# Performance work log

Measured on AMD Instinct MI355X. Metric: run time of the kernel, lower is better.

Reference implementation:

```python
import jax, jax.numpy as jnp
import numpy as np
from jax import lax

# --- fixed architecture (from init_kwargs) ---
S = 2048          # seq_len
HID = 2048        # hidden size
NH = 16           # num value heads == num key heads (v_per_k = 1)
DK = 128          # key head dim
DV = 128          # value head dim
K = 4             # depthwise conv kernel size
CS = 64           # chunk size
NC = S // CS      # number of chunks
KEY_DIM = NH * DK
VAL_DIM = NH * DV
CONV_DIM = 2 * KEY_DIM + VAL_DIM
EPS = 1e-6        # rms_norm_eps


def setup_inputs() -> dict:
    key = jax.random.key(0)
    ks = jax.random.split(key, 10)
    def n(k, shape, s=1.0):
        return s * jax.random.normal(k, shape, dtype=jnp.float32)
    return {
        'hidden_in':     n(ks[0], (1, S, HID)),
        'in_proj_qkv_w': n(ks[1], (CONV_DIM, HID), 0.02),
        'in_proj_z_w':   n(ks[2], (VAL_DIM, HID), 0.02),
        'in_proj_b_w':   n(ks[3], (NH, HID), 0.02),
        'in_proj_a_w':   n(ks[4], (NH, HID), 0.02),
        'out_proj_w':    n(ks[5], (HID, VAL_DIM), 0.02),
        'conv_w':        n(ks[6], (CONV_DIM, 1, K), 0.2),
        'dt_bias':       n(ks[7], (NH,), 0.1),
        'A_log':         n(ks[8], (NH,), 0.1),
        'norm_w':        1.0 + n(ks[9], (DV,), 0.02),
    }


def _l2norm(x):
    return x * lax.rsqrt(jnp.sum(x * x, axis=-1, keepdims=True) + 1e-6)


def _chunk_gated_delta_rule(q, k, v, g, beta):
    # q,k: (1,NH,S,DK)  v: (1,NH,S,DV)  g,beta: (1,NH,S)
    scale = 1.0 / np.sqrt(DK).astype(np.float32)
    q = q * scale
    kb = k * beta[..., None]
    vb = v * beta[..., None]
    q = q.reshape(1, NH, NC, CS, DK)
    k = k.reshape(1, NH, NC, CS, DK)
    v = v.reshape(1, NH, NC, CS, DV)
    kb = kb.reshape(1, NH, NC, CS, DK)
    vb = vb.reshape(1, NH, NC, CS, DV)
    g = jnp.cumsum(g.reshape(1, NH, NC, CS), axis=-1)

    gd = jnp.minimum(g[..., :, None] - g[..., None, :], 10.0)       # (1,NH,NC,CS,CS)
    tril = jnp.tril(jnp.ones((CS, CS), bool))                        # incl diag
    strict_low = jnp.tril(jnp.ones((CS, CS), bool), -1)
    dm = jnp.where(tril, jnp.exp(gd), 0.0)                           # decay mask

    # L = strictly-lower part of -(k_beta k^T) * decay_mask
    L = jnp.where(strict_low, -jnp.einsum('bhcid,bhcjd->bhcij', kb, k) * dm, 0.0)
    eye = jnp.eye(CS, dtype=q.dtype)

    # 64-step Neumann series inverting (I - L), with clamping as in source
    def neumann(attn, _):
        attn = eye + jnp.einsum('bhcij,bhcjk->bhcik', L, attn)
        return jnp.clip(attn, -1000.0, 1000.0), None
    attn, _ = lax.scan(neumann, jnp.broadcast_to(eye, L.shape), None, length=CS)

    value = jnp.einsum('bhcij,bhcjd->bhcid', attn, vb)
    kcd = jnp.einsum('bhcij,bhcjd->bhcid', attn, kb * jnp.exp(g)[..., None])

    xs = tuple(jnp.moveaxis(t, 2, 0) for t in (q, k, value, kcd, g, dm))

    def step(state, xs_i):  # state: (1,NH,DK,DV)
        qi, ki, vi, kcdi, gi, dmi = xs_i  # chunk tensors (1,NH,CS,...)
        ai = jnp.where(tril, jnp.einsum('bhid,bhjd->bhij', qi, ki) * dmi, 0.0)
        v_new = vi - jnp.einsum('bhid,bhdv->bhiv', kcdi, state)
        out_i = (jnp.einsum('bhid,bhdv->bhiv', qi * jnp.exp(gi)[..., None], state)
                 + jnp.einsum('bhij,bhjv->bhiv', ai, v_new))
        g_last = gi[..., -1:]                                        # (1,NH,1)
        state = (state * jnp.exp(g_last)[..., None]
                 + jnp.einsum('bhid,bhiv->bhdv', ki * jnp.exp(g_last - gi)[..., None], v_new))
        return state, out_i

    state0 = jnp.zeros((1, NH, DK, DV), q.dtype)
    last_state, outs = lax.scan(step, state0, xs)                    # outs: (NC,1,NH,CS,DV)
    core = jnp.moveaxis(outs, 0, 2).reshape(1, NH, S, DV)
    return core, last_state


def _forward(hidden_in, qkv_w, z_w, b_w, a_w, o_w, conv_w, dt_bias, A_log, norm_w):
    mixed = jnp.einsum('bsh,oh->bso', hidden_in, qkv_w)              # (1,S,CONV_DIM)
    z = jnp.einsum('bsh,oh->bso', hidden_in, z_w)                    # (1,S,VAL_DIM)
    b = jnp.einsum('bsh,oh->bso', hidden_in, b_w)                    # (1,S,NH)
    a = jnp.einsum('bsh,oh->bso', hidden_in, a_w)                    # (1,S,NH)

    # causal depthwise conv1d (padding=K-1 then truncate == left-pad K-1)
    x = jnp.pad(jnp.swapaxes(mixed, 1, 2), ((0, 0), (0, 0), (K - 1, 0)))
    conv = lax.conv_general_dilated(x, conv_w, (1,), 'VALID',
                                    dimension_numbers=('NCH', 'OIH', 'NCH'),
                                    feature_group_count=CONV_DIM)
    mixed = jax.nn.silu(jnp.swapaxes(conv, 1, 2))                    # (1,S,CONV_DIM)

    q = mixed[..., :KEY_DIM]
    k = mixed[..., KEY_DIM:2 * KEY_DIM]
    v = mixed[..., 2 * KEY_DIM:]
    q = _l2norm(jnp.swapaxes(q.reshape(1, S, NH, DK), 1, 2))         # (1,NH,S,DK)
    k = _l2norm(jnp.swapaxes(k.reshape(1, S, NH, DK), 1, 2))
    v = jnp.swapaxes(v.reshape(1, S, NH, DV), 1, 2)                  # (1,NH,S,DV)
    beta = jnp.swapaxes(jax.nn.sigmoid(b), 1, 2)                     # (1,NH,S)
    g = jnp.swapaxes(-jnp.exp(A_log) * jax.nn.softplus(a + dt_bias), 1, 2)

    core, _ = _chunk_gated_delta_rule(q, k, v, g, beta)              # (1,NH,S,DV)

    core_f = jnp.swapaxes(core, 1, 2).reshape(-1, DV)                # (S*NH, DV)
    z_f = z.reshape(-1, DV)
    # ANE rmsnorm trick == plain RMSNorm: x / sqrt(mean(x^2)+eps)
    xn = core_f * lax.rsqrt(jnp.mean(core_f * core_f, axis=-1, keepdims=True) + EPS) * norm_w
    out = (xn * jax.nn.silu(z_f)).reshape(1, S, VAL_DIM)
    return jnp.einsum('bsv,hv->bsh', out, o_w)


def reference(hidden_in, in_proj_qkv_w, in_proj_z_w, in_proj_b_w, in_proj_a_w,
              out_proj_w, conv_w, dt_bias, A_log, norm_w):
    return _forward(hidden_in, in_proj_qkv_w, in_proj_z_w, in_proj_b_w, in_proj_a_w,
                    out_proj_w, conv_w, dt_bias, A_log, norm_w)
```

## Files before the change

kernel.cpp:

```cpp
#include <hip/hip_runtime.h>
#include <math.h>

#define S_LEN 2048
#define HID 2048
#define NH 16
#define DK 128
#define DV 128
#define CS 64
#define NC 32
#define KEY_DIM 2048
#define VAL_DIM 2048
#define CONV_DIM 6144
#define QSCALE 0.08838834764831845f

typedef unsigned short u16;
typedef unsigned int u32;
typedef __bf16 bf16x8 __attribute__((ext_vector_type(8)));
typedef float f32x4 __attribute__((ext_vector_type(4)));

__device__ __forceinline__ float sigmoidf_(float x){ return 1.f/(1.f+expf(-x)); }
__device__ __forceinline__ u16 f2bf(float x){
  u32 u = __float_as_uint(x);
  return (u16)((u + 0x7fffu + ((u>>16)&1u)) >> 16);
}

constexpr size_t OFF_HIDBF  = 0;
constexpr size_t OFF_QKVWBF = 2097152;
constexpr size_t OFF_ZWBF   = 8388608;
constexpr size_t OFF_OWBF   = 10485760;
constexpr size_t OFF_GATED  = 12582912;
constexpr size_t OFF_MIXED  = 14680064;
constexpr size_t OFF_CONVO  = 27262976;
constexpr size_t OFF_Z      = 39845888;
constexpr size_t OFF_BRAW   = 44040192;
constexpr size_t OFF_ARAW   = 44072960;
constexpr size_t OFF_BETA   = 44105728;
constexpr size_t OFF_G      = 44138496;
constexpr size_t OFF_KCD    = 44171264;
constexpr size_t OFF_AI     = 48365568;
constexpr size_t OFF_SALL   = 50462720;
constexpr size_t OFF_CORE   = 58851328;
constexpr size_t OFF_AT     = OFF_MIXED;
constexpr size_t OFF_BM     = 0;
constexpr size_t OFF_BAPART = OFF_MIXED;

__global__ __launch_bounds__(256) void k_cast8(const float* __restrict__ in,
                                               u16* __restrict__ out, int n8)
{
  int i = blockIdx.x*256 + threadIdx.x;
  if (i >= n8) return;
  const float4 a = *(const float4*)(in + (size_t)i*8);
  const float4 b = *(const float4*)(in + (size_t)i*8 + 4);
  uint4 o;
  o.x = (u32)f2bf(a.x) | ((u32)f2bf(a.y)<<16);
  o.y = (u32)f2bf(a.z) | ((u32)f2bf(a.w)<<16);
  o.z = (u32)f2bf(b.x) | ((u32)f2bf(b.y)<<16);
  o.w = (u32)f2bf(b.z) | ((u32)f2bf(b.w)<<16);
  *(uint4*)(out + (size_t)i*8) = o;
}

__device__ __forceinline__ void gload16(const u16* g, u16* l){
  __builtin_amdgcn_global_load_lds(
      (__attribute__((address_space(1))) void*)(void*)g,
      (__attribute__((address_space(3))) void*)l, 16, 0, 0);
}

__global__ __launch_bounds__(256) void gemm_bf(const u16* __restrict__ A,
    const u16* __restrict__ B, float* __restrict__ C, int M, int N, int Kd)
{
  __shared__ u16 As[128*32];
  __shared__ u16 Bs[128*32];
  const int tid = threadIdx.x;
  const int w = tid>>6, lane = tid&63;
  const int wr = w>>1, wc = w&1;
  const int row0 = blockIdx.y*128, col0 = blockIdx.x*128;

  f32x4 acc[4][4] = {};

  const int sr = lane>>2;
  const int sk = (lane&3)*8;
  const u16* Ag0 = A + (size_t)(row0 + (2*w  )*16 + sr)*Kd + sk;
  const u16* Ag1 = A + (size_t)(row0 + (2*w+1)*16 + sr)*Kd + sk;
  const u16* Bg0 = B + (size_t)(col0 + (2*w  )*16 + sr)*Kd + sk;
  const u16* Bg1 = B + (size_t)(col0 + (2*w+1)*16 + sr)*Kd + sk;
  u16* Al0 = &As[(2*w  )*16*32];
  u16* Al1 = &As[(2*w+1)*16*32];
  u16* Bl0 = &Bs[(2*w  )*16*32];
  u16* Bl1 = &Bs[(2*w+1)*16*32];

  const int fr = lane&15, fc = (lane>>4)*8;
  const int arow0 = (wr*64 + fr)*32 + fc;
  const int brow0 = (wc*64 + fr)*32 + fc;

  for (int k0=0; k0<Kd; k0+=32){
    __syncthreads();
    gload16(Ag0 + k0, Al0);
    gload16(Ag1 + k0, Al1);
    gload16(Bg0 + k0, Bl0);
    gload16(Bg1 + k0, Bl1);
    __syncthreads();
    bf16x8 af[4], bfr[4];
#pragma unroll
    for (int m=0;m<4;m++) af[m]  = *(const bf16x8*)&As[arow0 + m*16*32];
#pragma unroll
    for (int n=0;n<4;n++) bfr[n] = *(const bf16x8*)&Bs[brow0 + n*16*32];
#pragma unroll
    for (int m=0;m<4;m++)
#pragma unroll
      for (int n=0;n<4;n++)
        acc[m][n] = __builtin_amdgcn_mfma_f32_16x16x32_bf16(af[m], bfr[n], acc[m][n], 0,0,0);
  }

  const int cr = (lane>>4)*4, cc = lane&15;
#pragma unroll
  for (int m=0;m<4;m++)
#pragma unroll
    for (int n=0;n<4;n++){
      float* cp = C + (size_t)(row0 + wr*64 + m*16 + cr)*N + (col0 + wc*64 + n*16 + cc);
#pragma unroll
      for (int j=0;j<4;j++) cp[(size_t)j*N] = acc[m][n][j];
    }
}

#define BA_KS 512
__global__ __launch_bounds__(256) void k_ba_part(const float* __restrict__ hid,
  const float* __restrict__ bw, const float* __restrict__ aw, float* __restrict__ part)
{
  __shared__ float Ash[32][132];
  __shared__ float Wsh[32][132];
  const int t = threadIdx.x;
  const int ty = t>>4, tx = t&15;
  const int s0 = blockIdx.x*32;
  const int k00 = blockIdx.y*BA_KS;
  float acc[2][2] = {{0.f,0.f},{0.f,0.f}};
#pragma unroll 1
  for (int kt=0; kt<BA_KS; kt+=128){
    const int k0 = k00 + kt;
    __syncthreads();
#pragma unroll
    for (int q=0;q<4;q++){
      int idx = t + q*256;
      int r = idx>>5, c4 = (idx&31)*4;
      *(float4*)&Ash[r][c4] = *(const float4*)&hid[(size_t)(s0+r)*HID + k0 + c4];
      const float* wrow = (r<16)? (bw + (size_t)r*HID) : (aw + (size_t)(r-16)*HID);
      *(float4*)&Wsh[r][c4] = *(const float4*)&wrow[k0 + c4];
    }
    __syncthreads();
#pragma unroll
    for (int kq=0;kq<32;kq++){
      float4 a0 = *(const float4*)&Ash[ty*2  ][kq*4];
      float4 a1 = *(const float4*)&Ash[ty*2+1][kq*4];
      float4 w0 = *(const float4*)&Wsh[tx*2  ][kq*4];
      float4 w1 = *(const float4*)&Wsh[tx*2+1][kq*4];
      acc[0][0] += a0.x*w0.x + a0.y*w0.y + a0.z*w0.z + a0.w*w0.w;
      acc[0][1] += a0.x*w1.x + a0.y*w1.y + a0.z*w1.z + a0.w*w1.w;
      acc[1][0] += a1.x*w0.x + a1.y*w0.y + a1.z*w0.z + a1.w*w0.w;
      acc[1][1] += a1.x*w1.x + a1.y*w1.y + a1.z*w1.z + a1.w*w1.w;
    }
  }
  float* pb = part + (size_t)blockIdx.y*S_LEN*32;
#pragma unroll
  for (int i=0;i<2;i++)
#pragma unroll
    for (int j=0;j<2;j++)
      pb[(size_t)(s0+ty*2+i)*32 + tx*2+j] = acc[i][j];
}

__global__ __launch_bounds__(256) void k_ba_red(const float* __restrict__ part,
  float* __restrict__ braw, float* __restrict__ araw)
{
  int idx = blockIdx.x*256 + threadIdx.x;
  if (idx >= S_LEN*32) return;
  float v = part[idx] + part[idx + S_LEN*32] + part[idx + 2*S_LEN*32] + part[idx + 3*S_LEN*32];
  int s = idx>>5, o = idx&31;
  if (o<16) braw[s*NH+o] = v; else araw[s*NH+(o-16)] = v;
}

__global__ __launch_bounds__(64) void k_beta_g(const float* __restrict__ braw,
  const float* __restrict__ araw, const float* __restrict__ dtb,
  const float* __restrict__ alog, float* __restrict__ beta, float* __restrict__ G)
{
  const int b = blockIdx.x;
  const int n = b & (NH-1), c = b >> 4;
  const int t = threadIdx.x;
  const int s = c*CS + t;
  float x = araw[s*NH+n] + dtb[n];
  float sp = (x > 20.f) ? x : log1pf(expf(x));
  float g = -expf(alog[n]) * sp;
#pragma unroll
  for (int off=1; off<64; off<<=1){
    float u = __shfl_up(g, off, 64);
    if (t >= off) g += u;
  }
  G[s*NH+n] = g;
  float bb = braw[s*NH+n];
  beta[s*NH+n] = 1.f/(1.f+expf(-bb));
}

__global__ __launch_bounds__(256) void k_conv(const float* __restrict__ mixed,
  const float* __restrict__ cw, float* __restrict__ convo)
{
  const int ch = blockIdx.x*256 + threadIdx.x;
  const int s0 = blockIdx.y*4;
  const float w0=cw[ch*4], w1=cw[ch*4+1], w2=cw[ch*4+2], w3=cw[ch*4+3];
  float m[7];
#pragma unroll
  for (int j=0;j<7;j++){
    int s = s0 + j - 3;
    m[j] = (s>=0) ? mixed[(size_t)s*CONV_DIM+ch] : 0.f;
  }
#pragma unroll
  for (int i=0;i<4;i++){
    float acc = m[i]*w0 + m[i+1]*w1 + m[i+2]*w2 + m[i+3]*w3;
    convo[(size_t)(s0+i)*CONV_DIM+ch] = acc*sigmoidf_(acc);
  }
}

__global__ __launch_bounds__(256) void k_l2norm(float* __restrict__ convo)
{
  const int t = threadIdx.x;
  const int lane = t & 63, w = t >> 6;
  const int s = blockIdx.x;
  const int n = blockIdx.y*4 + w;
  {
    float* q = convo + (size_t)s*CONV_DIM + n*DK;
    float q0 = q[lane], q1 = q[lane+64];
    float ss = q0*q0 + q1*q1;
#pragma unroll
    for (int m=1;m<64;m<<=1) ss += __shfl_xor(ss, m, 64);
    float r = rsqrtf(ss + 1e-6f) * QSCALE;
    q[lane] = q0*r; q[lane+64] = q1*r;
  }
  {
    float* k = convo + (size_t)s*CONV_DIM + KEY_DIM + n*DK;
    float k0 = k[lane], k1 = k[lane+64];
    float ss = k0*k0 + k1*k1;
#pragma unroll
    for (int m=1;m<64;m<<=1) ss += __shfl_xor(ss, m, 64);
    float r = rsqrtf(ss + 1e-6f);
    k[lane] = k0*r; k[lane+64] = k1*r;
  }
}

__global__ __launch_bounds__(256) void k_chunk1(float* __restrict__ convo,
  const float* __restrict__ G, const float* __restrict__ beta,
  float* __restrict__ ai_g, float* __restrict__ kcd_g)
{
  __shared__ float KT[128][76];
  __shared__ float LT[64][65];
  __shared__ float reds[4][64];
  __shared__ float Gs[64], bets[64], kes[64];
  const int c = blockIdx.x, n = blockIdx.y;
  const int t = threadIdx.x;
  const int tx = t & 15, ty = t >> 4;
  const int s0 = c*CS;
  if (t < 64){
    float gv = G[(s0+t)*NH+n], bv = beta[(s0+t)*NH+n];
    Gs[t]=gv; bets[t]=bv; kes[t]=bv*expf(gv);
  }
  __syncthreads();
  for (int idx=t; idx<CS*DK; idx+=256){
    int i = idx>>7, d = idx&127;
    KT[d][i] = convo[(size_t)(s0+i)*CONV_DIM + KEY_DIM + n*DK + d];
  }
  __syncthreads();
  {
    const int i0=ty*4, j0=tx*4;
    float l[4][4]={};
    for (int d=0; d<DK; d++){
      float4 ki = *(const float4*)&KT[d][i0];
      float4 kj = *(const float4*)&KT[d][j0];
      float kiv[4]={ki.x,ki.y,ki.z,ki.w};
      float kjv[4]={kj.x,kj.y,kj.z,kj.w};
#pragma unroll
      for (int a=0;a<4;a++)
#pragma unroll
        for (int b=0;b<4;b++) l[a][b] += kiv[a]*kjv[b];
    }
#pragma unroll
    for (int a=0;a<4;a++)
#pragma unroll
      for (int b=0;b<4;b++){
        int i=i0+a, j=j0+b;
        LT[i][j] = (j<i) ? (-bets[i]*l[a][b]*expf(fminf(Gs[i]-Gs[j],10.f))) : 0.f;
      }
  }
  __syncthreads();
  {
    const int i0=ty*4, j0=tx*4;
    float acc[4][4]={};
    for (int d=0; d<DK; d++){
      float4 kj = *(const float4*)&KT[d][j0];
      float kjv[4]={kj.x,kj.y,kj.z,kj.w};
      float qv[4];
#pragma unroll
      for (int a=0;a<4;a++) qv[a] = convo[(size_t)(s0+i0+a)*CONV_DIM + n*DK + d];
#pragma unroll
      for (int a=0;a<4;a++)
#pragma unroll
        for (int b=0;b<4;b++) acc[a][b] += qv[a]*kjv[b];
    }
    size_t ab = ((size_t)(n*NC+c))*CS*CS;
#pragma unroll
    for (int a=0;a<4;a++)
#pragma unroll
      for (int b=0;b<4;b++){
        int i=i0+a, j=j0+b;
        ai_g[ab + i*CS + j] = (j<=i) ? acc[a][b]*expf(fminf(Gs[i]-Gs[j],10.f)) : 0.f;
      }
  }
  __syncthreads();
  if (t==0) LT[0][0]=1.f;
  __syncthreads();
#pragma unroll 1
  for (int i=1;i<64;i++){
    const int j = t&63, pg = t>>6;
    float part=0.f;
    if (j < i){
      for (int p=j+1+pg; p<i; p+=4) part += LT[i][p]*LT[p][j];
    }
    reds[pg][j]=part;
    __syncthreads();
    if (t < 64){
      if (t < i) LT[i][t] += reds[0][t]+reds[1][t]+reds[2][t]+reds[3][t];
      else if (t==i) LT[i][i] = 1.f;
    }
    __syncthreads();
  }
  {
    const int i0=ty*4, d0=tx*8;
    float acc[4][8]={};
    for (int p=0;p<CS;p++){
      float lt[4];
#pragma unroll
      for (int a=0;a<4;a++) lt[a]=LT[i0+a][p];
      const float bp = bets[p];
      const float* vr = convo + (size_t)(s0+p)*CONV_DIM + 2*KEY_DIM + n*DV + d0;
      float4 v0=*(const float4*)vr, v1=*(const float4*)(vr+4);
      float vv[8]={v0.x*bp,v0.y*bp,v0.z*bp,v0.w*bp,v1.x*bp,v1.y*bp,v1.z*bp,v1.w*bp};
#pragma unroll
      for (int a=0;a<4;a++)
#pragma unroll
        for (int b=0;b<8;b++) acc[a][b] += lt[a]*vv[b];
    }
    __syncthreads();
#pragma unroll
    for (int a=0;a<4;a++){
      float* orow = convo + (size_t)(s0+i0+a)*CONV_DIM + 2*KEY_DIM + n*DV + d0;
      *(float4*)orow     = make_float4(acc[a][0],acc[a][1],acc[a][2],acc[a][3]);
      *(float4*)(orow+4) = make_float4(acc[a][4],acc[a][5],acc[a][6],acc[a][7]);
    }
  }
  {
    const int i0=(t&7)*8, d0=(t>>3)*4;
    float acc[8][4]={};
    for (int p=0;p<CS;p++){
      const float ke = kes[p];
      float lt[8];
#pragma unroll
      for (int a=0;a<8;a++) lt[a]=LT[i0+a][p];
      float kv[4];
#pragma unroll
      for (int b=0;b<4;b++) kv[b]=KT[d0+b][p]*ke;
#pragma unroll
      for (int a=0;a<8;a++)
#pragma unroll
        for (int b=0;b<4;b++) acc[a][b]+=lt[a]*kv[b];
    }
    size_t kb = ((size_t)(n*NC+c))*CS*DK;
#pragma unroll
    for (int a=0;a<8;a++)
      *(float4*)&kcd_g[kb + (size_t)(i0+a)*DK + d0] =
          make_float4(acc[a][0],acc[a][1],acc[a][2],acc[a][3]);
  }
}

__global__ __launch_bounds__(256) void k_chunk2(const float* __restrict__ convo,
  const float* __restrict__ kcd_g, const float* __restrict__ G,
  float* __restrict__ AT_g, float* __restrict__ B_g)
{
  __shared__ float Ks[32][132], Cs[32][132], Vs[32][132];
  __shared__ float Gsh[64];
  const int c = blockIdx.x, n = blockIdx.y;
  const int t = threadIdx.x;
  const int tx = t&15, ty = t>>4;
  if (t<64) Gsh[t] = G[(c*CS+t)*NH+n];
  __syncthreads();
  const float gl = Gsh[63];
  float accA[8][8]={}, accB[8][8]={};
#pragma unroll 1
  for (int ib=0; ib<2; ib++){
    __syncthreads();
    for (int fi=t; fi<32*32; fi+=256){
      int i = fi>>5, dq=(fi&31)*4;
      int sg = c*CS + ib*32 + i;
      float ef = expf(gl - Gsh[ib*32+i]);
      float4 kv = *(const float4*)&convo[(size_t)sg*CONV_DIM + KEY_DIM + n*DK + dq];
      *(float4*)&Ks[i][dq] = make_float4(kv.x*ef,kv.y*ef,kv.z*ef,kv.w*ef);
      *(float4*)&Cs[i][dq] = *(const float4*)&kcd_g[((size_t)(n*NC+c)*CS + ib*32+i)*DK + dq];
      *(float4*)&Vs[i][dq] = *(const float4*)&convo[(size_t)sg*CONV_DIM + 2*KEY_DIM + n*DV + dq];
    }
    __syncthreads();
    for (int i=0;i<32;i++){
      float krx[8], cpy[8], kry[8], vdx[8];
      float4 u,v;
      u=*(const float4*)&Ks[i][tx*4]; v=*(const float4*)&Ks[i][64+tx*4];
      krx[0]=u.x;krx[1]=u.y;krx[2]=u.z;krx[3]=u.w;krx[4]=v.x;krx[5]=v.y;krx[6]=v.z;krx[7]=v.w;
      u=*(const float4*)&Cs[i][ty*4]; v=*(const float4*)&Cs[i][64+ty*4];
      cpy[0]=u.x;cpy[1]=u.y;cpy[2]=u.z;cpy[3]=u.w;cpy[4]=v.x;cpy[5]=v.y;cpy[6]=v.z;cpy[7]=v.w;
      u=*(const float4*)&Ks[i][ty*4]; v=*(const float4*)&Ks[i][64+ty*4];
      kry[0]=u.x;kry[1]=u.y;kry[2]=u.z;kry[3]=u.w;kry[4]=v.x;kry[5]=v.y;kry[6]=v.z;kry[7]=v.w;
      u=*(const float4*)&Vs[i][tx*4]; v=*(const float4*)&Vs[i][64+tx*4];
      vdx[0]=u.x;vdx[1]=u.y;vdx[2]=u.z;vdx[3]=u.w;vdx[4]=v.x;vdx[5]=v.y;vdx[6]=v.z;vdx[7]=v.w;
#pragma unroll
      for (int a=0;a<8;a++)
#pragma unroll
        for (int b=0;b<8;b++){
          accA[a][b] += cpy[a]*krx[b];
          accB[a][b] += kry[a]*vdx[b];
        }
    }
  }
  const float egl = expf(gl);
  const size_t ab = (size_t)(n*NC+c)*DK*DK;
#pragma unroll
  for (int a=0;a<8;a++){
    int p = (a<4)?(ty*4+a):(64+ty*4+a-4);
#pragma unroll
    for (int bq=0;bq<2;bq++){
      int r0 = (bq==0)?(tx*4):(64+tx*4);
      float o[4];
#pragma unroll
      for (int j=0;j<4;j++){
        int r = r0+j;
        float val = -accA[a][bq*4+j];
        if (p==r) val += egl;
        o[j]=val;
      }
      *(float4*)&AT_g[ab + (size_t)p*DK + r0] = make_float4(o[0],o[1],o[2],o[3]);
    }
  }
  const size_t bb = (size_t)(n*NC+c)*DK*DV;
#pragma unroll
  for (int a=0;a<8;a++){
    int r = (a<4)?(ty*4+a):(64+ty*4+a-4);
#pragma unroll
    for (int bq=0;bq<2;bq++){
      int d0 = (bq==0)?(tx*4):(64+tx*4);
      *(float4*)&B_g[bb + (size_t)r*DV + d0] =
        make_float4(accB[a][bq*4+0],accB[a][bq*4+1],accB[a][bq*4+2],accB[a][bq*4+3]);
    }
  }
}

__global__ __launch_bounds__(256) void k_scan(const float* __restrict__ AT_g,
  const float* __restrict__ B_g, float* __restrict__ Sall)
{
  __shared__ float Ash[64][132];
  __shared__ float SL[128][20];
  const int n = blockIdx.x, cg = blockIdx.y;
  const int t = threadIdx.x;
  const int r0 = (t&63)*2, d0 = (t>>6)*4;
  for (int idx=t; idx<128*20; idx+=256) (&SL[0][0])[idx]=0.f;
  __syncthreads();
#pragma unroll 1
  for (int c=0;c<NC;c++){
    const size_t mb = (size_t)(n*NC+c)*DK;
#pragma unroll
    for (int rr=0;rr<2;rr++){
      float4 sv = *(float4*)&SL[r0+rr][d0];
      *(float4*)&Sall[(mb + r0+rr)*DV + cg*16 + d0] = sv;
    }
    float acc[2][4]={};
#pragma unroll 1
    for (int pb=0;pb<2;pb++){
      __syncthreads();
      const size_t abase = (mb + pb*64)*DK;
#pragma unroll
      for (int q=0;q<8;q++){
        int fi = t + q*256;
        int p = fi>>5, rq=(fi&31)*4;
        *(float4*)&Ash[p][rq] = *(const float4*)&AT_g[abase + (size_t)p*DK + rq];
      }
      __syncthreads();
      for (int pp=0;pp<64;pp++){
        float a0=Ash[pp][r0], a1=Ash[pp][r0+1];
        float4 sv=*(float4*)&SL[pb*64+pp][d0];
        float s4[4]={sv.x,sv.y,sv.z,sv.w};
#pragma unroll
        for (int dd=0;dd<4;dd++){ acc[0][dd]+=a0*s4[dd]; acc[1][dd]+=a1*s4[dd]; }
      }
    }
    __syncthreads();
    float4 b0=*(const float4*)&B_g[(mb + r0)*DV + cg*16 + d0];
    float4 b1=*(const float4*)&B_g[(mb + r0+1)*DV + cg*16 + d0];
    float4 n0=make_float4(acc[0][0]+b0.x, acc[0][1]+b0.y, acc[0][2]+b0.z, acc[0][3]+b0.w);
    float4 n1=make_float4(acc[1][0]+b1.x, acc[1][1]+b1.y, acc[1][2]+b1.z, acc[1][3]+b1.w);
    *(float4*)&SL[r0][d0]=n0; *(float4*)&SL[r0+1][d0]=n1;
    __syncthreads();
  }
}

__global__ __launch_bounds__(256) void k_out(const float* __restrict__ convo,
  const float* __restrict__ kcd_g, const float* __restrict__ ai_g,
  const float* __restrict__ Sall, const float* __restrict__ G,
  float* __restrict__ core)
{
  __shared__ float Ssh[32][132];
  __shared__ float Wsh[64][132];
  __shared__ float egs[64];
  const int c = blockIdx.x, n = blockIdx.y;
  const int t = threadIdx.x;
  const int tx = t&15, ty = t>>4;
  const int i0 = ty*4, d0 = tx*8;
  const int s0 = c*CS;
  if (t<64) egs[t] = expf(G[(s0+t)*NH+n]);
  float wacc[4][8]={}, oacc[4][8]={};
  const size_t mb = (size_t)(n*NC+c)*DK;
  const size_t kb = (size_t)(n*NC+c)*CS*DK;
#pragma unroll 1
  for (int rb=0;rb<4;rb++){
    __syncthreads();
    for (int fi=t; fi<32*32; fi+=256){
      int rr=fi>>5, dq=(fi&31)*4;
      *(float4*)&Ssh[rr][dq] = *(const float4*)&Sall[(mb + rb*32+rr)*DV + dq];
    }
    __syncthreads();
    for (int r2=0;r2<32;r2++){
      int r = rb*32+r2;
      float4 sa=*(const float4*)&Ssh[r2][d0], sb=*(const float4*)&Ssh[r2][d0+4];
      float sv[8]={sa.x,sa.y,sa.z,sa.w,sb.x,sb.y,sb.z,sb.w};
      float qv[4], kv[4];
#pragma unroll
      for (int a=0;a<4;a++){
        qv[a] = convo[(size_t)(s0+i0+a)*CONV_DIM + n*DK + r] * egs[i0+a];
        kv[a] = kcd_g[kb + (size_t)(i0+a)*DK + r];
      }
#pragma unroll
      for (int a=0;a<4;a++)
#pragma unroll
        for (int b=0;b<8;b++){
          oacc[a][b] += qv[a]*sv[b];
          wacc[a][b] += kv[a]*sv[b];
        }
    }
  }
  __syncthreads();
#pragma unroll
  for (int a=0;a<4;a++){
    const float* vr = convo + (size_t)(s0+i0+a)*CONV_DIM + 2*KEY_DIM + n*DV + d0;
    float4 v0=*(const float4*)vr, v1=*(const float4*)(vr+4);
    *(float4*)&Wsh[i0+a][d0]   = make_float4(v0.x-wacc[a][0],v0.y-wacc[a][1],v0.z-wacc[a][2],v0.w-wacc[a][3]);
    *(float4*)&Wsh[i0+a][d0+4] = make_float4(v1.x-wacc[a][4],v1.y-wacc[a][5],v1.z-wacc[a][6],v1.w-wacc[a][7]);
  }
  __syncthreads();
  const size_t aib = (size_t)(n*NC+c)*CS*CS;
  for (int j=0;j<CS;j++){
    float4 w0=*(const float4*)&Wsh[j][d0], w1=*(const float4*)&Wsh[j][d0+4];
    float wv[8]={w0.x,w0.y,w0.z,w0.w,w1.x,w1.y,w1.z,w1.w};
    float av[4];
#pragma unroll
    for (int a=0;a<4;a++) av[a]=ai_g[aib + (size_t)(i0+a)*CS + j];
#pragma unroll
    for (int a=0;a<4;a++)
#pragma unroll
      for (int b=0;b<8;b++) oacc[a][b]+=av[a]*wv[b];
  }
#pragma unroll
  for (int a=0;a<4;a++){
    float* cr = core + (size_t)(s0+i0+a)*VAL_DIM + n*DV + d0;
    *(float4*)cr     = make_float4(oacc[a][0],oacc[a][1],oacc[a][2],oacc[a][3]);
    *(float4*)(cr+4) = make_float4(oacc[a][4],oacc[a][5],oacc[a][6],oacc[a][7]);
  }
}

__global__ __launch_bounds__(256) void k_norm_gate(const float* __restrict__ core,
  const float* __restrict__ z, const float* __restrict__ nw, u16* __restrict__ gated)
{
  const int t=threadIdx.x, lane=t&63, w=t>>6;
  const int row = blockIdx.x*4 + w;
  const float* cr = core + (size_t)row*DV;
  float c0=cr[lane], c1=cr[lane+64];
  float ss=c0*c0+c1*c1;
#pragma unroll
  for (int m=1;m<64;m<<=1) ss += __shfl_xor(ss,m,64);
  float sc = rsqrtf(ss*(1.f/128.f) + 1e-6f);
  const float* zr = z + (size_t)row*DV;
  float z0=zr[lane], z1=zr[lane+64];
  u16* gr = gated + (size_t)row*DV;
  gr[lane]    = f2bf(c0*sc*nw[lane]    * (z0*sigmoidf_(z0)));
  gr[lane+64] = f2bf(c1*sc*nw[lane+64] * (z1*sigmoidf_(z1)));
}

extern "C" void kernel_launch(void* const* d_in, const int* in_sizes, int n_in,
                              void* d_out, int out_size, void* d_ws, size_t ws_size,
                              hipStream_t stream)
{
  (void)in_sizes; (void)n_in; (void)out_size; (void)ws_size;
  const float* hid  = (const float*)d_in[0];
  const float* qkvw = (const float*)d_in[1];
  const float* zw   = (const float*)d_in[2];
  const float* bw   = (const float*)d_in[3];
  const float* aw   = (const float*)d_in[4];
  const float* ow   = (const float*)d_in[5];
  const float* cw   = (const float*)d_in[6];
  const float* dtb  = (const float*)d_in[7];
  const float* alog = (const float*)d_in[8];
  const float* nw   = (const float*)d_in[9];

  float* ws     = (float*)d_ws;
  u16* hid_bf   = (u16*)(ws + OFF_HIDBF);
  u16* qkvw_bf  = (u16*)(ws + OFF_QKVWBF);
  u16* zw_bf    = (u16*)(ws + OFF_ZWBF);
  u16* ow_bf    = (u16*)(ws + OFF_OWBF);
  u16* gated_bf = (u16*)(ws + OFF_GATED);
  float* mixed  = ws + OFF_MIXED;
  float* convo  = ws + OFF_CONVO;
  float* zbuf   = ws + OFF_Z;
  float* braw   = ws + OFF_BRAW;
  float* araw   = ws + OFF_ARAW;
  float* beta   = ws + OFF_BETA;
  float* G      = ws + OFF_G;
  float* kcd    = ws + OFF_KCD;
  float* ai     = ws + OFF_AI;
  float* AT     = ws + OFF_AT;
  float* Bm     = ws + OFF_BM;
  float* Sall   = ws + OFF_SALL;
  float* core   = ws + OFF_CORE;
  float* bapart = ws + OFF_BAPART;

  k_ba_part<<<dim3(S_LEN/32, 4), 256, 0, stream>>>(hid, bw, aw, bapart);
  k_ba_red<<<(S_LEN*32+255)/256, 256, 0, stream>>>(bapart, braw, araw);
  k_beta_g<<<NH*NC, 64, 0, stream>>>(braw, araw, dtb, alog, beta, G);

  k_cast8<<<(S_LEN*HID/8+255)/256,    256, 0, stream>>>(hid,  hid_bf,  S_LEN*HID/8);
  k_cast8<<<(CONV_DIM*HID/8+255)/256, 256, 0, stream>>>(qkvw, qkvw_bf, CONV_DIM*HID/8);
  k_cast8<<<(VAL_DIM*HID/8+255)/256,  256, 0, stream>>>(zw,   zw_bf,   VAL_DIM*HID/8);
  k_cast8<<<(HID*VAL_DIM/8+255)/256,  256, 0, stream>>>(ow,   ow_bf,   HID*VAL_DIM/8);

  gemm_bf<<<dim3(CONV_DIM/128, S_LEN/128), 256, 0, stream>>>(hid_bf, qkvw_bf, mixed, S_LEN, CONV_DIM, HID);
  gemm_bf<<<dim3(VAL_DIM/128,  S_LEN/128), 256, 0, stream>>>(hid_bf, zw_bf,   zbuf,  S_LEN, VAL_DIM, HID);
  k_conv<<<dim3(CONV_DIM/256, S_LEN/4), 256, 0, stream>>>(mixed, cw, convo);
  k_l2norm<<<dim3(S_LEN, NH/4), 256, 0, stream>>>(convo);
  k_chunk1<<<dim3(NC, NH), 256, 0, stream>>>(convo, G, beta, ai, kcd);
  k_chunk2<<<dim3(NC, NH), 256, 0, stream>>>(convo, kcd, G, AT, Bm);
  k_scan<<<dim3(NH, 8), 256, 0, stream>>>(AT, Bm, Sall);
  k_out<<<dim3(NC, NH), 256, 0, stream>>>(convo, kcd, ai, Sall, G, core);
  k_norm_gate<<<S_LEN*NH/4, 256, 0, stream>>>(core, zbuf, nw, gated_bf);
  gemm_bf<<<dim3(HID/128, S_LEN/128), 256, 0, stream>>>(gated_bf, ow_bf, (float*)d_out, S_LEN, HID, VAL_DIM);
}
```

Before: 578.4 us.

## Replace affine-map state scan with direct recurrent delta-rule scan

The old path built dense 128x128 per-chunk transition matrices (A = egl*I - kcd^T k~) plus B matrices in k_chunk2 and scanned them with matrix-matrix products. The new k_scan2 drops k_chunk2 and runs the recurrence directly: per chunk it computes v_new = v - kcd·S, stores it, then updates S = egl*S + k~^T v_new. It prefetches the next chunk's operands into registers and double-buffers the decayed keys in shared memory. k_out now reads the precomputed v_new instead of recomputing it. This cuts large matrix writes and FLOPs, at the cost of a longer serial per-chunk chain split across 16 column groups per head.

```diff
diff --git a/kernel.cpp b/kernel.cpp
--- a/kernel.cpp
+++ b/kernel.cpp
@@ -40,9 +40,9 @@
 constexpr size_t OFF_AI     = 48365568;
 constexpr size_t OFF_SALL   = 50462720;
 constexpr size_t OFF_CORE   = 58851328;
-constexpr size_t OFF_AT     = OFF_MIXED;
-constexpr size_t OFF_BM     = 0;
 constexpr size_t OFF_BAPART = OFF_MIXED;
+constexpr size_t OFF_KTIL   = OFF_MIXED;
+constexpr size_t OFF_VNEW   = 0;
 
 __global__ __launch_bounds__(256) void k_cast8(const float* __restrict__ in,
                                                u16* __restrict__ out, int n8)
@@ -244,12 +244,12 @@
 
 __global__ __launch_bounds__(256) void k_chunk1(float* __restrict__ convo,
   const float* __restrict__ G, const float* __restrict__ beta,
-  float* __restrict__ ai_g, float* __restrict__ kcd_g)
+  float* __restrict__ ai_g, float* __restrict__ kcd_g, float* __restrict__ ktil_g)
 {
   __shared__ float KT[128][76];
   __shared__ float LT[64][65];
   __shared__ float reds[4][64];
-  __shared__ float Gs[64], bets[64], kes[64];
+  __shared__ float Gs[64], bets[64], kes[64], eds_s[64];
   const int c = blockIdx.x, n = blockIdx.y;
   const int t = threadIdx.x;
   const int tx = t & 15, ty = t >> 4;
@@ -259,6 +259,7 @@
     Gs[t]=gv; bets[t]=bv; kes[t]=bv*expf(gv);
   }
   __syncthreads();
+  if (t < 64) eds_s[t] = expf(Gs[63]-Gs[t]);
   for (int idx=t; idx<CS*DK; idx+=256){
     int i = idx>>7, d = idx&127;
     KT[d][i] = convo[(size_t)(s0+i)*CONV_DIM + KEY_DIM + n*DK + d];
@@ -372,137 +373,106 @@
     for (int a=0;a<8;a++)
       *(float4*)&kcd_g[kb + (size_t)(i0+a)*DK + d0] =
           make_float4(acc[a][0],acc[a][1],acc[a][2],acc[a][3]);
-  }
-}
-
-__global__ __launch_bounds__(256) void k_chunk2(const float* __restrict__ convo,
-  const float* __restrict__ kcd_g, const float* __restrict__ G,
-  float* __restrict__ AT_g, float* __restrict__ B_g)
-{
-  __shared__ float Ks[32][132], Cs[32][132], Vs[32][132];
-  __shared__ float Gsh[64];
-  const int c = blockIdx.x, n = blockIdx.y;
-  const int t = threadIdx.x;
-  const int tx = t&15, ty = t>>4;
-  if (t<64) Gsh[t] = G[(c*CS+t)*NH+n];
-  __syncthreads();
-  const float gl = Gsh[63];
-  float accA[8][8]={}, accB[8][8]={};
-#pragma unroll 1
-  for (int ib=0; ib<2; ib++){
-    __syncthreads();
-    for (int fi=t; fi<32*32; fi+=256){
-      int i = fi>>5, dq=(fi&31)*4;
-      int sg = c*CS + ib*32 + i;
-      float ef = expf(gl - Gsh[ib*32+i]);
-      float4 kv = *(const float4*)&convo[(size_t)sg*CONV_DIM + KEY_DIM + n*DK + dq];
-      *(float4*)&Ks[i][dq] = make_float4(kv.x*ef,kv.y*ef,kv.z*ef,kv.w*ef);
-      *(float4*)&Cs[i][dq] = *(const float4*)&kcd_g[((size_t)(n*NC+c)*CS + ib*32+i)*DK + dq];
-      *(float4*)&Vs[i][dq] = *(const float4*)&convo[(size_t)sg*CONV_DIM + 2*KEY_DIM + n*DV + dq];
-    }
-    __syncthreads();
-    for (int i=0;i<32;i++){
-      float krx[8], cpy[8], kry[8], vdx[8];
-      float4 u,v;
-      u=*(const float4*)&Ks[i][tx*4]; v=*(const float4*)&Ks[i][64+tx*4];
-      krx[0]=u.x;krx[1]=u.y;krx[2]=u.z;krx[3]=u.w;krx[4]=v.x;krx[5]=v.y;krx[6]=v.z;krx[7]=v.w;
-      u=*(const float4*)&Cs[i][ty*4]; v=*(const float4*)&Cs[i][64+ty*4];
-      cpy[0]=u.x;cpy[1]=u.y;cpy[2]=u.z;cpy[3]=u.w;cpy[4]=v.x;cpy[5]=v.y;cpy[6]=v.z;cpy[7]=v.w;
-      u=*(const float4*)&Ks[i][ty*4]; v=*(const float4*)&Ks[i][64+ty*4];
-      kry[0]=u.x;kry[1]=u.y;kry[2]=u.z;kry[3]=u.w;kry[4]=v.x;kry[5]=v.y;kry[6]=v.z;kry[7]=v.w;
-      u=*(const float4*)&Vs[i][tx*4]; v=*(const float4*)&Vs[i][64+tx*4];
-      vdx[0]=u.x;vdx[1]=u.y;vdx[2]=u.z;vdx[3]=u.w;vdx[4]=v.x;vdx[5]=v.y;vdx[6]=v.z;vdx[7]=v.w;
-#pragma unroll
-      for (int a=0;a<8;a++)
-#pragma unroll
-        for (int b=0;b<8;b++){
-          accA[a][b] += cpy[a]*krx[b];
-          accB[a][b] += kry[a]*vdx[b];
-        }
-    }
-  }
-  const float egl = expf(gl);
-  const size_t ab = (size_t)(n*NC+c)*DK*DK;
-#pragma unroll
-  for (int a=0;a<8;a++){
-    int p = (a<4)?(ty*4+a):(64+ty*4+a-4);
-#pragma unroll
-    for (int bq=0;bq<2;bq++){
-      int r0 = (bq==0)?(tx*4):(64+tx*4);
-      float o[4];
-#pragma unroll
-      for (int j=0;j<4;j++){
-        int r = r0+j;
-        float val = -accA[a][bq*4+j];
-        if (p==r) val += egl;
-        o[j]=val;
-      }
-      *(float4*)&AT_g[ab + (size_t)p*DK + r0] = make_float4(o[0],o[1],o[2],o[3]);
-    }
-  }
-  const size_t bb = (size_t)(n*NC+c)*DK*DV;
-#pragma unroll
-  for (int a=0;a<8;a++){
-    int r = (a<4)?(ty*4+a):(64+ty*4+a-4);
-#pragma unroll
-    for (int bq=0;bq<2;bq++){
-      int d0 = (bq==0)?(tx*4):(64+tx*4);
-      *(float4*)&B_g[bb + (size_t)r*DV + d0] =
-        make_float4(accB[a][bq*4+0],accB[a][bq*4+1],accB[a][bq*4+2],accB[a][bq*4+3]);
-    }
-  }
-}
-
-__global__ __launch_bounds__(256) void k_scan(const float* __restrict__ AT_g,
-  const float* __restrict__ B_g, float* __restrict__ Sall)
-{
-  __shared__ float Ash[64][132];
-  __shared__ float SL[128][20];
+#pragma unroll
+    for (int a=0;a<8;a++){
+      float ed = eds_s[i0+a];
+      *(float4*)&ktil_g[kb + (size_t)(i0+a)*DK + d0] = make_float4(
+        KT[d0][i0+a]*ed, KT[d0+1][i0+a]*ed, KT[d0+2][i0+a]*ed, KT[d0+3][i0+a]*ed);
+    }
+  }
+}
+
+#define CG 16
+__global__ __launch_bounds__(256,1) void k_scan2(
+  const float* __restrict__ convo, const float* __restrict__ kcd_g,
+  const float* __restrict__ ktil_g, const float* __restrict__ G,
+  float* __restrict__ Sall, float* __restrict__ vnew)
+{
+  __shared__ float S[128][12];
+  __shared__ float Kt[2][64][130];
+  __shared__ float Vs[64][12];
+  __shared__ float Wp[4][64][12];
   const int n = blockIdx.x, cg = blockIdx.y;
   const int t = threadIdx.x;
-  const int r0 = (t&63)*2, d0 = (t>>6)*4;
-  for (int idx=t; idx<128*20; idx+=256) (&SL[0][0])[idx]=0.f;
-  __syncthreads();
+  const int li = t & 63, pg = t >> 6;
+  const int ur = t & 127, uh = t >> 7;
+  const int d0 = cg*8;
+  const int ki = t>>2, kr = (t&3)*32;
+
+  for (int idx=t; idx<128*12; idx+=256) (&S[0][0])[idx]=0.f;
+
+  float4 ktn[8], kcn[8];
+  float2 valn;
+  {
+    const size_t kb = ((size_t)(n*NC))*CS*DK;
+#pragma unroll
+    for (int j=0;j<8;j++) ktn[j] = *(const float4*)&ktil_g[kb + (size_t)ki*DK + kr + j*4];
+#pragma unroll
+    for (int j=0;j<8;j++) kcn[j] = *(const float4*)&kcd_g[kb + (size_t)li*DK + pg*32 + j*4];
+    valn = *(const float2*)&convo[(size_t)li*CONV_DIM + 2*KEY_DIM + n*DV + d0 + pg*2];
+  }
+  __syncthreads();
+
 #pragma unroll 1
   for (int c=0;c<NC;c++){
+    const int s0 = c*CS;
+    const int buf = c&1;
+#pragma unroll
+    for (int j=0;j<8;j++){
+      *(float2*)&Kt[buf][ki][kr + j*4]     = make_float2(ktn[j].x, ktn[j].y);
+      *(float2*)&Kt[buf][ki][kr + j*4 + 2] = make_float2(ktn[j].z, ktn[j].w);
+    }
     const size_t mb = (size_t)(n*NC+c)*DK;
-#pragma unroll
-    for (int rr=0;rr<2;rr++){
-      float4 sv = *(float4*)&SL[r0+rr][d0];
-      *(float4*)&Sall[(mb + r0+rr)*DV + cg*16 + d0] = sv;
-    }
-    float acc[2][4]={};
-#pragma unroll 1
-    for (int pb=0;pb<2;pb++){
-      __syncthreads();
-      const size_t abase = (mb + pb*64)*DK;
-#pragma unroll
-      for (int q=0;q<8;q++){
-        int fi = t + q*256;
-        int p = fi>>5, rq=(fi&31)*4;
-        *(float4*)&Ash[p][rq] = *(const float4*)&AT_g[abase + (size_t)p*DK + rq];
+    {
+      float4 sv = *(float4*)&S[ur][uh*4];
+      *(float4*)&Sall[(mb + ur)*DV + d0 + uh*4] = sv;
+    }
+    float w0=0,w1=0,w2=0,w3=0,w4=0,w5=0,w6=0,w7=0;
+#pragma unroll
+    for (int q=0;q<8;q++){
+      float kq[4] = {kcn[q].x,kcn[q].y,kcn[q].z,kcn[q].w};
+#pragma unroll
+      for (int e=0;e<4;e++){
+        int r = pg*32 + q*4 + e;
+        float4 sa = *(float4*)&S[r][0];
+        float4 sb = *(float4*)&S[r][4];
+        w0 += kq[e]*sa.x; w1 += kq[e]*sa.y; w2 += kq[e]*sa.z; w3 += kq[e]*sa.w;
+        w4 += kq[e]*sb.x; w5 += kq[e]*sb.y; w6 += kq[e]*sb.z; w7 += kq[e]*sb.w;
       }
-      __syncthreads();
-      for (int pp=0;pp<64;pp++){
-        float a0=Ash[pp][r0], a1=Ash[pp][r0+1];
-        float4 sv=*(float4*)&SL[pb*64+pp][d0];
-        float s4[4]={sv.x,sv.y,sv.z,sv.w};
-#pragma unroll
-        for (int dd=0;dd<4;dd++){ acc[0][dd]+=a0*s4[dd]; acc[1][dd]+=a1*s4[dd]; }
+    }
+    *(float4*)&Wp[pg][li][0] = make_float4(w0,w1,w2,w3);
+    *(float4*)&Wp[pg][li][4] = make_float4(w4,w5,w6,w7);
+    const int cn = (c+1<NC)?(c+1):c;
+    const size_t kbn = ((size_t)(n*NC+cn))*CS*DK;
+#pragma unroll
+    for (int j=0;j<8;j++) ktn[j] = *(const float4*)&ktil_g[kbn + (size_t)ki*DK + kr + j*4];
+#pragma unroll
+    for (int j=0;j<8;j++) kcn[j] = *(const float4*)&kcd_g[kbn + (size_t)li*DK + pg*32 + j*4];
+    __syncthreads();
+    float vn0 = valn.x - (Wp[0][li][pg*2  ]+Wp[1][li][pg*2  ]+Wp[2][li][pg*2  ]+Wp[3][li][pg*2  ]);
+    float vn1 = valn.y - (Wp[0][li][pg*2+1]+Wp[1][li][pg*2+1]+Wp[2][li][pg*2+1]+Wp[3][li][pg*2+1]);
+    *(float2*)&Vs[li][pg*2] = make_float2(vn0,vn1);
+    *(float2*)&vnew[((size_t)(n*NC+c)*CS + li)*DV + d0 + pg*2] = make_float2(vn0,vn1);
+    valn = *(const float2*)&convo[(size_t)(cn*CS+li)*CONV_DIM + 2*KEY_DIM + n*DV + d0 + pg*2];
+    const float egl = expf(G[(s0+CS-1)*NH + n]);
+    __syncthreads();
+    {
+      float4 sv = *(float4*)&S[ur][uh*4];
+      float a0=sv.x*egl, a1=sv.y*egl, a2=sv.z*egl, a3=sv.w*egl;
+#pragma unroll
+      for (int i=0;i<64;i++){
+        float kt = Kt[buf][i][ur];
+        float4 vb = *(float4*)&Vs[i][uh*4];
+        a0 += kt*vb.x; a1 += kt*vb.y; a2 += kt*vb.z; a3 += kt*vb.w;
       }
-    }
-    __syncthreads();
-    float4 b0=*(const float4*)&B_g[(mb + r0)*DV + cg*16 + d0];
-    float4 b1=*(const float4*)&B_g[(mb + r0+1)*DV + cg*16 + d0];
-    float4 n0=make_float4(acc[0][0]+b0.x, acc[0][1]+b0.y, acc[0][2]+b0.z, acc[0][3]+b0.w);
-    float4 n1=make_float4(acc[1][0]+b1.x, acc[1][1]+b1.y, acc[1][2]+b1.z, acc[1][3]+b1.w);
-    *(float4*)&SL[r0][d0]=n0; *(float4*)&SL[r0+1][d0]=n1;
+      *(float4*)&S[ur][uh*4] = make_float4(a0,a1,a2,a3);
+    }
     __syncthreads();
   }
 }
 
 __global__ __launch_bounds__(256) void k_out(const float* __restrict__ convo,
-  const float* __restrict__ kcd_g, const float* __restrict__ ai_g,
+  const float* __restrict__ vnew, const float* __restrict__ ai_g,
   const float* __restrict__ Sall, const float* __restrict__ G,
   float* __restrict__ core)
 {
@@ -515,9 +485,15 @@
   const int i0 = ty*4, d0 = tx*8;
   const int s0 = c*CS;
   if (t<64) egs[t] = expf(G[(s0+t)*NH+n]);
-  float wacc[4][8]={}, oacc[4][8]={};
+  __syncthreads();
+  for (int fi=t; fi<64*32; fi+=256){
+    int i=fi>>5, rq=(fi&31)*4;
+    float4 qv = *(const float4*)&convo[(size_t)(s0+i)*CONV_DIM + n*DK + rq];
+    float e = egs[i];
+    *(float4*)&Wsh[i][rq] = make_float4(qv.x*e,qv.y*e,qv.z*e,qv.w*e);
+  }
+  float oacc[4][8]={};
   const size_t mb = (size_t)(n*NC+c)*DK;
-  const size_t kb = (size_t)(n*NC+c)*CS*DK;
 #pragma unroll 1
   for (int rb=0;rb<4;rb++){
     __syncthreads();
@@ -530,28 +506,19 @@
       int r = rb*32+r2;
       float4 sa=*(const float4*)&Ssh[r2][d0], sb=*(const float4*)&Ssh[r2][d0+4];
       float sv[8]={sa.x,sa.y,sa.z,sa.w,sb.x,sb.y,sb.z,sb.w};
-      float qv[4], kv[4];
-#pragma unroll
-      for (int a=0;a<4;a++){
-        qv[a] = convo[(size_t)(s0+i0+a)*CONV_DIM + n*DK + r] * egs[i0+a];
-        kv[a] = kcd_g[kb + (size_t)(i0+a)*DK + r];
-      }
+      float qv[4];
+#pragma unroll
+      for (int a=0;a<4;a++) qv[a] = Wsh[i0+a][r];
 #pragma unroll
       for (int a=0;a<4;a++)
 #pragma unroll
-        for (int b=0;b<8;b++){
-          oacc[a][b] += qv[a]*sv[b];
-          wacc[a][b] += kv[a]*sv[b];
-        }
-    }
-  }
-  __syncthreads();
-#pragma unroll
-  for (int a=0;a<4;a++){
-    const float* vr = convo + (size_t)(s0+i0+a)*CONV_DIM + 2*KEY_DIM + n*DV + d0;
-    float4 v0=*(const float4*)vr, v1=*(const float4*)(vr+4);
-    *(float4*)&Wsh[i0+a][d0]   = make_float4(v0.x-wacc[a][0],v0.y-wacc[a][1],v0.z-wacc[a][2],v0.w-wacc[a][3]);
-    *(float4*)&Wsh[i0+a][d0+4] = make_float4(v1.x-wacc[a][4],v1.y-wacc[a][5],v1.z-wacc[a][6],v1.w-wacc[a][7]);
+        for (int b=0;b<8;b++) oacc[a][b] += qv[a]*sv[b];
+    }
+  }
+  __syncthreads();
+  for (int fi=t; fi<64*32; fi+=256){
+    int i=fi>>5, dq=(fi&31)*4;
+    *(float4*)&Wsh[i][dq] = *(const float4*)&vnew[((size_t)(n*NC+c)*CS + i)*DV + dq];
   }
   __syncthreads();
   const size_t aib = (size_t)(n*NC+c)*CS*CS;
@@ -623,11 +590,11 @@
   float* G      = ws + OFF_G;
   float* kcd    = ws + OFF_KCD;
   float* ai     = ws + OFF_AI;
-  float* AT     = ws + OFF_AT;
-  float* Bm     = ws + OFF_BM;
   float* Sall   = ws + OFF_SALL;
   float* core   = ws + OFF_CORE;
   float* bapart = ws + OFF_BAPART;
+  float* ktil   = ws + OFF_KTIL;
+  float* vnew   = ws + OFF_VNEW;
 
   k_ba_part<<<dim3(S_LEN/32, 4), 256, 0, stream>>>(hid, bw, aw, bapart);
   k_ba_red<<<(S_LEN*32+255)/256, 256, 0, stream>>>(bapart, braw, araw);
@@ -642,10 +609,9 @@
   gemm_bf<<<dim3(VAL_DIM/128,  S_LEN/128), 256, 0, stream>>>(hid_bf, zw_bf,   zbuf,  S_LEN, VAL_DIM, HID);
   k_conv<<<dim3(CONV_DIM/256, S_LEN/4), 256, 0, stream>>>(mixed, cw, convo);
   k_l2norm<<<dim3(S_LEN, NH/4), 256, 0, stream>>>(convo);
-  k_chunk1<<<dim3(NC, NH), 256, 0, stream>>>(convo, G, beta, ai, kcd);
-  k_chunk2<<<dim3(NC, NH), 256, 0, stream>>>(convo, kcd, G, AT, Bm);
-  k_scan<<<dim3(NH, 8), 256, 0, stream>>>(AT, Bm, Sall);
-  k_out<<<dim3(NC, NH), 256, 0, stream>>>(convo, kcd, ai, Sall, G, core);
+  k_chunk1<<<dim3(NC, NH), 256, 0, stream>>>(convo, G, beta, ai, kcd, ktil);
+  k_scan2<<<dim3(NH, CG), 256, 0, stream>>>(convo, kcd, ktil, G, Sall, vnew);
+  k_out<<<dim3(NC, NH), 256, 0, stream>>>(convo, vnew, ai, Sall, G, core);
   k_norm_gate<<<S_LEN*NH/4, 256, 0, stream>>>(core, zbuf, nw, gated_bf);
   gemm_bf<<<dim3(HID/128, S_LEN/128), 256, 0, stream>>>(gated_bf, ow_bf, (float*)d_out, S_LEN, HID, VAL_DIM);
 }
```

Result: faster. 497.0 us (-14.1%).
